# Optimization experiments

Measured on AMD Instinct MI355X. Metric: run time of the kernel, lower is better.

Reference implementation:

```python
import jax, jax.numpy as jnp
import numpy as np

E, TOPK, R = 8, 2, 16          # num_experts, top_k, rank_per_expert
D, H, GH = 1024, 16, 256       # embed_dim, num_heads, gating hidden
HD = D // H
SCALE = HD ** -0.5


def setup_inputs() -> dict:
    key = jax.random.key(0)
    ks = jax.random.split(key, 32)
    B, S = 32, 257
    inp = {"hidden_states": jax.random.normal(ks[0], (B, S, D), jnp.float32)}
    # gating network params
    inp["gw1"] = jax.random.normal(ks[1], (GH, D), jnp.float32) * 0.02
    inp["gb1"] = jnp.zeros((GH,), jnp.float32)
    inp["gw2"] = jax.random.normal(ks[2], (E, GH), jnp.float32) * 0.02
    inp["gb2"] = jnp.zeros((E,), jnp.float32)
    # four SVDMoeLinear projections: main weight, expert U/S/V, bias
    i = 3
    for p in ("q", "k", "v", "o"):
        inp[p + "Wm"] = jax.random.normal(ks[i], (D, D), jnp.float32) * 0.02; i += 1
        inp[p + "U"] = jax.random.normal(ks[i], (E, D, R), jnp.float32) * 0.02; i += 1
        inp[p + "S"] = jax.random.normal(ks[i], (E, R), jnp.float32) * 0.1; i += 1
        inp[p + "V"] = jax.random.normal(ks[i], (E, R, D), jnp.float32) * 0.02; i += 1
        inp[p + "b"] = jnp.zeros((D,), jnp.float32)
    return inp


def _svd_moe(x, Wm, U, S, V, b, idx, gates):
    # x: (B,S,D); idx,gates: (B,k); U:(E,D,R) S:(E,R) V:(E,R,D)
    main = jnp.einsum('bsd,od->bso', x, Wm)
    Ug, Sg, Vg = U[idx], S[idx], V[idx]        # (B,k,D,R), (B,k,R), (B,k,R,D)
    xv = jnp.einsum('bsd,bkrd->bksr', x, Vg)   # project into expert subspace
    xvs = xv * Sg[:, :, None, :]
    eo = jnp.einsum('bksr,bkor->bkso', xvs, Ug)
    expert = jnp.einsum('bkso,bk->bso', eo, gates)
    return main + expert + b


def reference(hidden_states, gw1, gb1, gw2, gb2,
              qWm, qU, qS, qV, qb,
              kWm, kU, kS, kV, kb,
              vWm, vU, vS, vV, vb,
              oWm, oU, oS, oV, ob):
    B, S, _ = hidden_states.shape
    # per-sample gating on pooled features
    pooled = hidden_states.mean(axis=1)
    h = jax.nn.relu(pooled @ gw1.T + gb1)
    logits = h @ gw2.T + gb2                    # (B,E)
    top_vals, top_idx = jax.lax.top_k(logits, TOPK)
    gates = jax.nn.softmax(top_vals, axis=-1)   # (B,k)

    q = _svd_moe(hidden_states, qWm, qU, qS, qV, qb, top_idx, gates) * SCALE
    k = _svd_moe(hidden_states, kWm, kU, kS, kV, kb, top_idx, gates)
    v = _svd_moe(hidden_states, vWm, vU, vS, vV, vb, top_idx, gates)

    def shp(t):
        return t.reshape(B, S, H, HD).transpose(0, 2, 1, 3)  # (B,H,S,HD)
    q, k, v = shp(q), shp(k), shp(v)
    attn = jax.nn.softmax(jnp.einsum('bhsd,bhtd->bhst', q, k), axis=-1)
    ctx = jnp.einsum('bhst,bhtd->bhsd', attn, v)
    ctx = ctx.transpose(0, 2, 1, 3).reshape(B, S, D)
    out = _svd_moe(ctx, oWm, oU, oS, oV, ob, top_idx, gates)
    return out
```

## Files before the change

kernel.cpp:

```cpp
#include <hip/hip_runtime.h>
#include <math.h>

#define Bb   32
#define SQ   257
#define SQV  320
#define Dm   1024
#define HD   64
#define Ee   8
#define Rr   16
#define GHh  256
#define NT   (Bb*SQ)
#define KX   1152
#define LDP  72

typedef unsigned short ush;
typedef _Float16 h16;
typedef __attribute__((ext_vector_type(8))) _Float16 half8;
typedef __attribute__((ext_vector_type(4))) _Float16 half4;
typedef __attribute__((ext_vector_type(8))) short short8;
typedef __attribute__((ext_vector_type(4))) float floatx4;
typedef __attribute__((ext_vector_type(16))) float floatx16;

__device__ __forceinline__ ush f2h(float f) {
    union { h16 h; ush u; } a; a.h = (h16)f; return a.u;
}
__device__ __forceinline__ void store_h4(ush* p, float4 v) {
    half4 h; h.x = (h16)v.x; h.y = (h16)v.y; h.z = (h16)v.z; h.w = (h16)v.w;
    *(half4*)p = h;
}
__device__ __forceinline__ void load16(const ush* g, ush* l) {
    __builtin_amdgcn_global_load_lds(
        (const __attribute__((address_space(1))) unsigned int*)g,
        (__attribute__((address_space(3))) unsigned int*)l,
        16, 0, 0);
}

__global__ __launch_bounds__(256) void prep_kernel(
    const float* __restrict__ x, float* __restrict__ pp, ush* __restrict__ xf,
    const float* __restrict__ W0, const float* __restrict__ U0,
    const float* __restrict__ W1, const float* __restrict__ U1,
    const float* __restrict__ W2, const float* __restrict__ U2,
    const float* __restrict__ W3, const float* __restrict__ U3,
    const float* __restrict__ V0, const float* __restrict__ V1,
    const float* __restrict__ V2, const float* __restrict__ V3,
    ush* __restrict__ Bf0, ush* __restrict__ Bf1,
    ush* __restrict__ Bf2, ush* __restrict__ Bf3,
    ush* __restrict__ Vf)
{
    const int bid = blockIdx.x, t = threadIdx.x;
    if (bid < 512) {
        const int c = bid & 15, b = bid >> 4;
        const int s0 = c * 16, s1 = (c == 15) ? SQ : s0 + 16;
        float4 acc = make_float4(0.f, 0.f, 0.f, 0.f);
        const float* xp = x + ((size_t)b * SQ + s0) * Dm + t * 4;
        ush* xo = xf + ((size_t)b * SQ + s0) * Dm + t * 4;
        for (int s = s0; s < s1; ++s, xp += Dm, xo += Dm) {
            float4 v = *(const float4*)xp;
            store_h4(xo, v);
            acc.x += v.x; acc.y += v.y; acc.z += v.z; acc.w += v.w;
        }
        *(float4*)(pp + ((size_t)b * 16 + c) * Dm + t * 4) = acc;
        return;
    }
    const int bx = bid - 512;
    const int p = bx / 1280, xb = bx % 1280;
    if (xb < 1152) {
        const float* W = p == 0 ? W0 : p == 1 ? W1 : p == 2 ? W2 : W3;
        const float* U = p == 0 ? U0 : p == 1 ? U1 : p == 2 ? U2 : U3;
        ush* Bf = p == 0 ? Bf0 : p == 1 ? Bf1 : p == 2 ? Bf2 : Bf3;
        const int i = xb * 256 + t;
        const int n = i / 288, c4 = i % 288, col = c4 * 4;
        float4 v;
        if (col < Dm) {
            v = *(const float4*)(W + (size_t)n * Dm + col);
        } else {
            int ec = col - Dm, e = ec >> 4, r = ec & 15;
            v = *(const float4*)(U + ((size_t)(e * Dm + n)) * Rr + r);
        }
        store_h4(Bf + (size_t)n * KX + col, v);
    } else {
        const float* V = p == 0 ? V0 : p == 1 ? V1 : p == 2 ? V2 : V3;
        const size_t i = ((size_t)(xb - 1152) * 256 + t) * 4;
        float4 v = *(const float4*)(V + i);
        store_h4(Vf + (size_t)p * Ee * Rr * Dm + i, v);
    }
}

__global__ __launch_bounds__(256) void gating_h(
    const float* __restrict__ pp, const float* __restrict__ gw1,
    const float* __restrict__ gb1, float* __restrict__ hbufg)
{
    __shared__ float pooled[Dm];
    const int b = blockIdx.x, slice = blockIdx.y, t = threadIdx.x;
    const int w = t >> 6, lane = t & 63;

    float4 acc = make_float4(0.f, 0.f, 0.f, 0.f);
    for (int c = 0; c < 16; ++c) {
        float4 v = *(const float4*)(pp + ((size_t)b * 16 + c) * Dm + t * 4);
        acc.x += v.x; acc.y += v.y; acc.z += v.z; acc.w += v.w;
    }
    const float sc = 1.0f / SQ;
    pooled[t*4+0] = acc.x * sc; pooled[t*4+1] = acc.y * sc;
    pooled[t*4+2] = acc.z * sc; pooled[t*4+3] = acc.w * sc;
    __syncthreads();

    for (int oi = 0; oi < 16; ++oi) {
        const int o = slice * 64 + w * 16 + oi;
        const float* g = gw1 + (size_t)o * Dm;
        float s = 0.f;
        #pragma unroll
        for (int i = 0; i < 16; ++i) s += pooled[lane + i*64] * g[lane + i*64];
        for (int off = 32; off > 0; off >>= 1) s += __shfl_down(s, off, 64);
        if (lane == 0) hbufg[b * GHh + o] = fmaxf(s + gb1[o], 0.f);
    }
}

__global__ __launch_bounds__(64) void gating_top(
    const float* __restrict__ hbufg, const float* __restrict__ gw2,
    const float* __restrict__ gb2,
    float* __restrict__ gates, int* __restrict__ idx)
{
    __shared__ float logits[Ee];
    const int b = blockIdx.x, t = threadIdx.x;
    if (t < Ee) {
        const float* g = gw2 + t * GHh;
        const float* hb = hbufg + b * GHh;
        float s = 0.f;
        for (int j = 0; j < GHh; ++j) s += hb[j] * g[j];
        logits[t] = s + gb2[t];
    }
    __syncthreads();
    if (t == 0) {
        int i1 = 0; float v1 = logits[0];
        for (int e = 1; e < Ee; ++e) if (logits[e] > v1) { v1 = logits[e]; i1 = e; }
        int i2 = 0; float v2 = -1e30f;
        for (int e = 0; e < Ee; ++e) if (e != i1 && logits[e] > v2) { v2 = logits[e]; i2 = e; }
        float e2 = __expf(v2 - v1);
        float inv = 1.f / (1.f + e2);
        gates[b*2+0] = inv; gates[b*2+1] = e2 * inv;
        idx[b*2+0] = i1; idx[b*2+1] = i2;
    }
}

template<int NP>
__global__ __launch_bounds__(256) void ext_gemm(
    const ush* __restrict__ xf,
    const ush* __restrict__ Vf,
    const float* __restrict__ S0, const float* __restrict__ S1,
    const float* __restrict__ S2,
    ush* __restrict__ o0, ush* __restrict__ o1, ush* __restrict__ o2,
    const float* __restrict__ gates, const int* __restrict__ idx, int pbase)
{
    __shared__ ush sA[2*64*32], sB[2*NP*16*32];
    const int mt = blockIdx.x, b = blockIdx.y, kk = blockIdx.z;
    const int t = threadIdx.x, lane = t & 63, w = t >> 6;
    const int quad = lane >> 4, l16 = lane & 15;
    const int s0 = mt * 64;
    const int e = idx[b*2+kk];
    const float g = gates[b*2+kk];

    if (kk == 0) {
        const int e0 = idx[b*2+0], e1 = idx[b*2+1];
        int zexp[6]; int nz = 0;
        #pragma unroll
        for (int ez = 0; ez < Ee; ++ez)
            if (ez != e0 && ez != e1) zexp[nz++] = ez;
        short8 zv = {0,0,0,0,0,0,0,0};
        for (int u = t; u < NP*64*6; u += 256) {
            const int ei = u % 6; int rest = u / 6;
            const int r64 = rest & 63; const int p = rest >> 6;
            const int s = s0 + r64;
            if (s < SQ) {
                ush* oo = p == 0 ? o0 : p == 1 ? o1 : o2;
                ush* dst = oo + ((size_t)(b*SQ + s)) * 128 + zexp[ei]*16;
                *(short8*)dst = zv;
                *(short8*)(dst + 8) = zv;
            }
        }
    }

    const int rl = lane >> 2;
    const int swsrc = ((lane & 3) ^ ((lane >> 3) & 3)) * 8;
    const int swrd  = ((quad ^ ((l16 >> 1) & 3)) * 8);

    int sa = s0 + w * 16 + rl; if (sa > SQ - 1) sa = SQ - 1;
    const ush* aptr = xf + ((size_t)(b * SQ + sa)) * Dm + swsrc;
    const ush* bptr = (w < NP)
        ? Vf + ((size_t)(pbase + w)) * Ee * Rr * Dm + ((size_t)(e * Rr + rl)) * Dm + swsrc
        : nullptr;
    ush* la0 = &sA[w * 512];
    ush* la1 = &sA[2048 + w * 512];
    ush* lb0 = (w < NP) ? &sB[w * 512] : nullptr;
    ush* lb1 = (w < NP) ? &sB[NP*512 + w * 512] : nullptr;

    floatx4 S[NP] = {};

    for (int it = 0; it < 16; ++it) {
        __syncthreads();
        load16(aptr, la0); load16(aptr + 32, la1); aptr += 64;
        if (w < NP) {
            load16(bptr, lb0); load16(bptr + 32, lb1); bptr += 64;
        }
        __syncthreads();
        #pragma unroll
        for (int j = 0; j < 2; ++j) {
            const half8 a = *(const half8*)&sA[j*2048 + (w*16 + l16)*32 + swrd];
            #pragma unroll
            for (int p = 0; p < NP; ++p) {
                const half8 bb = *(const half8*)&sB[j*NP*512 + (p*16 + l16)*32 + swrd];
                S[p] = __builtin_amdgcn_mfma_f32_16x16x32_f16(a, bb, S[p], 0, 0, 0);
            }
        }
    }

    #pragma unroll
    for (int p = 0; p < NP; ++p) {
        const float* Sp = p == 0 ? S0 : p == 1 ? S1 : S2;
        const float scale = g * Sp[e * Rr + l16];
        ush* oo = p == 0 ? o0 : p == 1 ? o1 : o2;
        #pragma unroll
        for (int r = 0; r < 4; ++r) {
            const int s = s0 + w * 16 + quad * 4 + r;
            if (s < SQ)
                oo[((size_t)(b * SQ + s)) * 128 + e * 16 + l16] = f2h(S[p][r] * scale);
        }
    }
}

template<int MODE>
__global__ __launch_bounds__(256) void gemm_mfma(
    const ush* __restrict__ A,
    const ush* __restrict__ E0, const ush* __restrict__ E1, const ush* __restrict__ E2,
    const ush* __restrict__ B0, const ush* __restrict__ B1, const ush* __restrict__ B2,
    const float* __restrict__ b0, const float* __restrict__ b1, const float* __restrict__ b2,
    ush* __restrict__ y0, ush* __restrict__ y1, ush* __restrict__ vt,
    float* __restrict__ yo, float qscale)
{
    const int stripe = blockIdx.x % 72;
    if (stripe >= 65) return;
    const int nb = blockIdx.x / 72;
    const int z = blockIdx.z;
    const ush* E = z == 0 ? E0 : z == 1 ? E1 : E2;
    const ush* Bm = z == 0 ? B0 : z == 1 ? B1 : B2;
    const float* bias = z == 0 ? b0 : z == 1 ? b1 : b2;

    __shared__ ush sLDS[2*128*64];
    ush* sA = sLDS;
    ush* sB = sLDS + 128*64;
    const int t = threadIdx.x, lane = t & 63, w = t >> 6;
    const int m0 = stripe * 128, n0 = nb * 128;
    const int row8 = lane >> 3, c8l = lane & 7;
    const int swk = (c8l ^ row8) * 8;
    const int wm = w >> 1, wn = w & 1;
    const int l31 = lane & 31, h5 = lane >> 5;

    const ush* ap[4]; const ush* ep[4]; const ush* bp[4];
    ush *la[4], *lb[4];
    #pragma unroll
    for (int c = 0; c < 4; ++c) {
        const int j = c * 4 + w;
        const int rowl = j * 8 + row8;
        int rga = m0 + rowl; if (rga > NT - 1) rga = NT - 1;
        ap[c] = A + (size_t)rga * Dm + swk;
        ep[c] = E + (size_t)rga * 128 + swk;
        bp[c] = Bm + (size_t)(n0 + rowl) * KX + swk;
        la[c] = &sA[j * 512];
        lb[c] = &sB[j * 512];
    }

    int aofs[4][2], bofs[4][2];
    #pragma unroll
    for (int s = 0; s < 4; ++s)
        #pragma unroll
        for (int i = 0; i < 2; ++i) {
            const int g = s * 2 + h5;
            aofs[s][i] = (wm*64 + i*32 + l31) * 64 + ((g ^ (l31 & 7)) * 8);
            bofs[s][i] = (wn*64 + i*32 + l31) * 64 + ((g ^ (l31 & 7)) * 8);
        }

    floatx16 acc[2][2] = {};

    for (int it = 0; it < 16; ++it) {
        __syncthreads();
        #pragma unroll
        for (int c = 0; c < 4; ++c) {
            load16(ap[c], la[c]); ap[c] += 64;
            load16(bp[c], lb[c]); bp[c] += 64;
        }
        __syncthreads();
        #pragma unroll
        for (int s = 0; s < 4; ++s) {
            half8 af0 = *(const half8*)&sA[aofs[s][0]];
            half8 af1 = *(const half8*)&sA[aofs[s][1]];
            half8 bf0 = *(const half8*)&sB[bofs[s][0]];
            half8 bf1 = *(const half8*)&sB[bofs[s][1]];
            acc[0][0] = __builtin_amdgcn_mfma_f32_32x32x16_f16(af0, bf0, acc[0][0], 0, 0, 0);
            acc[0][1] = __builtin_amdgcn_mfma_f32_32x32x16_f16(af0, bf1, acc[0][1], 0, 0, 0);
            acc[1][0] = __builtin_amdgcn_mfma_f32_32x32x16_f16(af1, bf0, acc[1][0], 0, 0, 0);
            acc[1][1] = __builtin_amdgcn_mfma_f32_32x32x16_f16(af1, bf1, acc[1][1], 0, 0, 0);
        }
    }
    for (int it = 0; it < 2; ++it) {
        __syncthreads();
        #pragma unroll
        for (int c = 0; c < 4; ++c) {
            load16(ep[c], la[c]); ep[c] += 64;
            load16(bp[c], lb[c]); bp[c] += 64;
        }
        __syncthreads();
        #pragma unroll
        for (int s = 0; s < 4; ++s) {
            half8 af0 = *(const half8*)&sA[aofs[s][0]];
            half8 af1 = *(const half8*)&sA[aofs[s][1]];
            half8 bf0 = *(const half8*)&sB[bofs[s][0]];
            half8 bf1 = *(const half8*)&sB[bofs[s][1]];
            acc[0][0] = __builtin_amdgcn_mfma_f32_32x32x16_f16(af0, bf0, acc[0][0], 0, 0, 0);
            acc[0][1] = __builtin_amdgcn_mfma_f32_32x32x16_f16(af0, bf1, acc[0][1], 0, 0, 0);
            acc[1][0] = __builtin_amdgcn_mfma_f32_32x32x16_f16(af1, bf0, acc[1][0], 0, 0, 0);
            acc[1][1] = __builtin_amdgcn_mfma_f32_32x32x16_f16(af1, bf1, acc[1][1], 0, 0, 0);
        }
    }

    if (MODE == 1) {
        #pragma unroll
        for (int mi = 0; mi < 2; ++mi) {
            #pragma unroll
            for (int ni = 0; ni < 2; ++ni) {
                const int col = n0 + wn*64 + ni*32 + l31;
                const float bsv = bias[col];
                const int rb = m0 + wm*64 + mi*32 + 4*h5;
                #pragma unroll
                for (int r = 0; r < 16; ++r) {
                    const int row = rb + (r & 3) + 8 * (r >> 2);
                    if (row < NT)
                        yo[(size_t)row * Dm + col] = acc[mi][ni][r] + bsv;
                }
            }
        }
    } else {
        __syncthreads();
        #pragma unroll
        for (int mi = 0; mi < 2; ++mi) {
            #pragma unroll
            for (int ni = 0; ni < 2; ++ni) {
                const int colL = wn*64 + ni*32 + l31;
                const float bsv = bias[n0 + colL];
                const int rbL = wm*64 + mi*32 + 4*h5;
                #pragma unroll
                for (int r = 0; r < 16; ++r) {
                    const int rowL = rbL + (r & 3) + 8 * (r >> 2);
                    float val = acc[mi][ni][r] + bsv;
                    if (z == 0) val *= qscale;
                    sLDS[rowL*128 + ((((colL>>3) ^ (rowL&7)) << 3) | (colL & 7))] = f2h(val);
                }
            }
        }
        __syncthreads();
        if (z != 2) {
            ush* y = (z == 0) ? y0 : y1;
            #pragma unroll
            for (int i = 0; i < 8; ++i) {
                const int u = i*256 + t;
                const int rowL = u >> 4, cj = u & 15;
                const int row = m0 + rowL;
                if (row < NT) {
                    half8 v = *(const half8*)&sLDS[rowL*128 + ((cj ^ (rowL&7)) << 3)];
                    *(half8*)(y + (size_t)row * Dm + n0 + cj*8) = v;
                }
            }
        } else {
            #pragma unroll
            for (int i = 0; i < 8; ++i) {
                const int u = i*256 + t;
                const int oct = u & 15, colL = u >> 4;
                const int colg = n0 + colL;
                const int h_ = colg >> 6, d_ = colg & 63;
                const size_t vrow = (size_t)h_ * 64 + d_;
                #pragma unroll
                for (int jj = 0; jj < 8; ++jj) {
                    const int rowL = oct + jj*16;
                    const int row = m0 + rowL;
                    if (row < NT) {
                        const int b_ = row / SQ, s_ = row - b_*SQ;
                        vt[((size_t)b_*1024 + vrow) * SQV + s_] =
                            sLDS[rowL*128 + ((((colL>>3) ^ (rowL&7)) << 3) | (colL & 7))];
                    }
                }
            }
        }
    }
}

__global__ __launch_bounds__(256) void attn_mfma(
    const ush* __restrict__ q, const ush* __restrict__ k,
    const ush* __restrict__ vt, ush* __restrict__ cf)
{
    __shared__ ush sK[64*LDP], sVt[64*LDP];
    __shared__ ush sP[4][16*LDP];
    const int qt = blockIdx.x, h = blockIdx.y, b = blockIdx.z;
    const int t = threadIdx.x, lane = t & 63, w = t >> 6;
    const int quad = lane >> 4, l16 = lane & 15;
    const size_t base = (size_t)b * SQ * Dm + (size_t)h * HD;
    const size_t vbase = ((size_t)(b * 16 + h)) * 64 * SQV;

    #pragma unroll
    for (int i = 0; i < 2; ++i) {
        const int u = t + i * 256;
        const int row = u >> 3, c8 = u & 7;
        int s = qt * 64 + row; if (s > SQ - 1) s = SQ - 1;
        short8 ld = *(const short8*)(q + base + (size_t)s * Dm + c8 * 8);
        *(short8*)&sK[row*LDP + c8*8] = ld;
    }
    __syncthreads();
    half8 qf[2];
    #pragma unroll
    for (int s = 0; s < 2; ++s)
        qf[s] = *(const half8*)&sK[(w*16 + l16)*LDP + s*32 + quad*8];

    floatx4 O[4] = {};
    float mrow[4], lrow[4];
    #pragma unroll
    for (int r = 0; r < 4; ++r) { mrow[r] = -1e30f; lrow[r] = 0.f; }
    const bool active = (qt * 64 + w * 16) < SQ;

    short8 kreg[2], vreg[2];
    auto prefetch = [&](int kt) {
        #pragma unroll
        for (int i = 0; i < 2; ++i) {
            const int u = t + i * 256;
            const int row = u >> 3, c8 = u & 7;
            const int s = kt * 64 + row;
            short8 kv = {0,0,0,0,0,0,0,0};
            if (s < SQ) kv = *(const short8*)(k + base + (size_t)s * Dm + c8 * 8);
            kreg[i] = kv;
            vreg[i] = *(const short8*)(vt + vbase + (size_t)row * SQV + kt*64 + c8*8);
        }
    };
    prefetch(0);

    for (int kt = 0; kt < 5; ++kt) {
        __syncthreads();
        #pragma unroll
        for (int i = 0; i < 2; ++i) {
            const int u = t + i * 256;
            const int row = u >> 3, c8 = u & 7;
            *(short8*)&sK[row*LDP + c8*8] = kreg[i];
            *(short8*)&sVt[row*LDP + c8*8] = vreg[i];
        }
        if (kt < 4) prefetch(kt + 1);
        __syncthreads();
        if (!active) continue;

        floatx4 S[4] = {};
        #pragma unroll
        for (int ni = 0; ni < 4; ++ni)
            #pragma unroll
            for (int s = 0; s < 2; ++s) {
                half8 kf = *(const half8*)&sK[(ni*16 + l16)*LDP + s*32 + quad*8];
                S[ni] = __builtin_amdgcn_mfma_f32_16x16x32_f16(qf[s], kf, S[ni], 0, 0, 0);
            }
        #pragma unroll
        for (int ni = 0; ni < 4; ++ni) {
            const int jg = kt * 64 + ni * 16 + l16;
            if (jg >= SQ) { S[ni][0] = -1e30f; S[ni][1] = -1e30f; S[ni][2] = -1e30f; S[ni][3] = -1e30f; }
        }
        float mnew[4], alpha[4];
        #pragma unroll
        for (int r = 0; r < 4; ++r) {
            float mx = fmaxf(fmaxf(S[0][r], S[1][r]), fmaxf(S[2][r], S[3][r]));
            #pragma unroll
            for (int off = 1; off < 16; off <<= 1) mx = fmaxf(mx, __shfl_xor(mx, off, 64));
            mnew[r] = fmaxf(mrow[r], mx);
            alpha[r] = __expf(mrow[r] - mnew[r]);
            mrow[r] = mnew[r];
        }
        float p[4][4], rs[4];
        #pragma unroll
        for (int r = 0; r < 4; ++r) rs[r] = 0.f;
        #pragma unroll
        for (int ni = 0; ni < 4; ++ni)
            #pragma unroll
            for (int r = 0; r < 4; ++r) {
                float e = __expf(S[ni][r] - mnew[r]);
                p[ni][r] = e; rs[r] += e;
            }
        #pragma unroll
        for (int r = 0; r < 4; ++r) {
            #pragma unroll
            for (int off = 1; off < 16; off <<= 1) rs[r] += __shfl_xor(rs[r], off, 64);
            lrow[r] = lrow[r] * alpha[r] + rs[r];
        }
        #pragma unroll
        for (int ni = 0; ni < 4; ++ni)
            #pragma unroll
            for (int r = 0; r < 4; ++r) O[ni][r] *= alpha[r];
        #pragma unroll
        for (int ni = 0; ni < 4; ++ni)
            #pragma unroll
            for (int r = 0; r < 4; ++r)
                sP[w][(quad*4 + r)*LDP + ni*16 + l16] = f2h(p[ni][r]);
        #pragma unroll
        for (int ni = 0; ni < 4; ++ni)
            #pragma unroll
            for (int s = 0; s < 2; ++s) {
                half8 a  = *(const half8*)&sP[w][l16*LDP + s*32 + quad*8];
                half8 bb = *(const half8*)&sVt[(ni*16 + l16)*LDP + s*32 + quad*8];
                O[ni] = __builtin_amdgcn_mfma_f32_16x16x32_f16(a, bb, O[ni], 0, 0, 0);
            }
    }

    if (active) {
        #pragma unroll
        for (int ni = 0; ni < 4; ++ni) {
            const int col = h * HD + ni * 16 + l16;
            #pragma unroll
            for (int r = 0; r < 4; ++r) {
                const int s = qt * 64 + w * 16 + quad * 4 + r;
                if (s < SQ)
                    cf[((size_t)(b * SQ + s)) * Dm + col] = f2h(O[ni][r] / lrow[r]);
            }
        }
    }
}

extern "C" void kernel_launch(void* const* d_in, const int* in_sizes, int n_in,
                              void* d_out, int out_size, void* d_ws, size_t ws_size,
                              hipStream_t stream)
{
    const float* x   = (const float*)d_in[0];
    const float* gw1 = (const float*)d_in[1];
    const float* gb1 = (const float*)d_in[2];
    const float* gw2 = (const float*)d_in[3];
    const float* gb2 = (const float*)d_in[4];
    const float *Wm[4], *U[4], *Sv[4], *Vv[4], *bias[4];
    for (int p = 0; p < 4; ++p) {
        Wm[p]   = (const float*)d_in[5 + p*5 + 0];
        U[p]    = (const float*)d_in[5 + p*5 + 1];
        Sv[p]   = (const float*)d_in[5 + p*5 + 2];
        Vv[p]   = (const float*)d_in[5 + p*5 + 3];
        bias[p] = (const float*)d_in[5 + p*5 + 4];
    }
    char* wsb   = (char*)d_ws;
    float* gates = (float*)wsb;
    int*   idx   = (int*)(wsb + 256);
    float* pool  = (float*)(wsb + 1024);
    float* hbufg = (float*)(wsb + 1024 + (size_t)Bb * 16 * Dm * 4);
    ush* p = (ush*)(wsb + 1024 + (size_t)Bb * 16 * Dm * 4 + (size_t)Bb * GHh * 4);
    ush* xf = p; p += (size_t)NT * Dm;
    ush* ef[4];
    for (int i = 0; i < 4; ++i) { ef[i] = p; p += (size_t)NT * 128; }
    ush* Bf[4];
    for (int i = 0; i < 4; ++i) { Bf[i] = p; p += (size_t)1024 * KX; }
    ush* Vf = p; p += (size_t)4 * Ee * Rr * Dm;
    ush* qf = p; p += (size_t)NT * Dm;
    ush* kf = p; p += (size_t)NT * Dm;
    ush* vt = p; p += (size_t)Bb * 16 * 64 * SQV;

    prep_kernel<<<5632, 256, 0, stream>>>(
        x, pool, xf,
        Wm[0], U[0], Wm[1], U[1], Wm[2], U[2], Wm[3], U[3],
        Vv[0], Vv[1], Vv[2], Vv[3],
        Bf[0], Bf[1], Bf[2], Bf[3], Vf);
    gating_h<<<dim3(Bb, 4), 256, 0, stream>>>(pool, gw1, gb1, hbufg);
    gating_top<<<Bb, 64, 0, stream>>>(hbufg, gw2, gb2, gates, idx);

    ext_gemm<3><<<dim3(5, Bb, 2), 256, 0, stream>>>(xf, Vf,
        Sv[0], Sv[1], Sv[2], ef[0], ef[1], ef[2], gates, idx, 0);

    gemm_mfma<0><<<dim3(576, 1, 3), 256, 0, stream>>>(
        xf, ef[0], ef[1], ef[2], Bf[0], Bf[1], Bf[2],
        bias[0], bias[1], bias[2], qf, kf, vt, nullptr, 0.125f);

    attn_mfma<<<dim3(5, 16, Bb), 256, 0, stream>>>(qf, kf, vt, xf);

    ext_gemm<1><<<dim3(5, Bb, 2), 256, 0, stream>>>(xf, Vf,
        Sv[3], Sv[3], Sv[3], ef[3], ef[3], ef[3], gates, idx, 3);

    gemm_mfma<1><<<dim3(576, 1, 1), 256, 0, stream>>>(
        xf, ef[3], ef[3], ef[3], Bf[3], Bf[3], Bf[3],
        bias[3], bias[3], bias[3], nullptr, nullptr, nullptr, (float*)d_out, 1.0f);
}
```

Baseline: 349.2 us.

## Load attention K/V fragments directly from global memory, drop LDS staging

```diff
diff --git a/kernel.cpp b/kernel.cpp
--- a/kernel.cpp
+++ b/kernel.cpp
@@ -104,8 +104,8 @@
     pooled[t*4+2] = acc.z * sc; pooled[t*4+3] = acc.w * sc;
     __syncthreads();
 
-    for (int oi = 0; oi < 16; ++oi) {
-        const int o = slice * 64 + w * 16 + oi;
+    for (int oi = 0; oi < 8; ++oi) {
+        const int o = slice * 32 + w * 8 + oi;
         const float* g = gw1 + (size_t)o * Dm;
         float s = 0.f;
         #pragma unroll
@@ -395,7 +395,6 @@
     const ush* __restrict__ q, const ush* __restrict__ k,
     const ush* __restrict__ vt, ush* __restrict__ cf)
 {
-    __shared__ ush sK[64*LDP], sVt[64*LDP];
     __shared__ ush sP[4][16*LDP];
     const int qt = blockIdx.x, h = blockIdx.y, b = blockIdx.z;
     const int t = threadIdx.x, lane = t & 63, w = t >> 6;
@@ -403,62 +402,34 @@
     const size_t base = (size_t)b * SQ * Dm + (size_t)h * HD;
     const size_t vbase = ((size_t)(b * 16 + h)) * 64 * SQV;
 
-    #pragma unroll
-    for (int i = 0; i < 2; ++i) {
-        const int u = t + i * 256;
-        const int row = u >> 3, c8 = u & 7;
-        int s = qt * 64 + row; if (s > SQ - 1) s = SQ - 1;
-        short8 ld = *(const short8*)(q + base + (size_t)s * Dm + c8 * 8);
-        *(short8*)&sK[row*LDP + c8*8] = ld;
-    }
-    __syncthreads();
+    if (qt * 64 + w * 16 >= SQ) return;
+
     half8 qf[2];
-    #pragma unroll
-    for (int s = 0; s < 2; ++s)
-        qf[s] = *(const half8*)&sK[(w*16 + l16)*LDP + s*32 + quad*8];
+    {
+        int r = qt * 64 + w * 16 + l16; if (r > SQ - 1) r = SQ - 1;
+        const ush* qp = q + base + (size_t)r * Dm;
+        #pragma unroll
+        for (int s = 0; s < 2; ++s)
+            qf[s] = *(const half8*)(qp + s * 32 + quad * 8);
+    }
 
     floatx4 O[4] = {};
     float mrow[4], lrow[4];
     #pragma unroll
     for (int r = 0; r < 4; ++r) { mrow[r] = -1e30f; lrow[r] = 0.f; }
-    const bool active = (qt * 64 + w * 16) < SQ;
-
-    short8 kreg[2], vreg[2];
-    auto prefetch = [&](int kt) {
-        #pragma unroll
-        for (int i = 0; i < 2; ++i) {
-            const int u = t + i * 256;
-            const int row = u >> 3, c8 = u & 7;
-            const int s = kt * 64 + row;
-            short8 kv = {0,0,0,0,0,0,0,0};
-            if (s < SQ) kv = *(const short8*)(k + base + (size_t)s * Dm + c8 * 8);
-            kreg[i] = kv;
-            vreg[i] = *(const short8*)(vt + vbase + (size_t)row * SQV + kt*64 + c8*8);
-        }
-    };
-    prefetch(0);
 
     for (int kt = 0; kt < 5; ++kt) {
-        __syncthreads();
-        #pragma unroll
-        for (int i = 0; i < 2; ++i) {
-            const int u = t + i * 256;
-            const int row = u >> 3, c8 = u & 7;
-            *(short8*)&sK[row*LDP + c8*8] = kreg[i];
-            *(short8*)&sVt[row*LDP + c8*8] = vreg[i];
-        }
-        if (kt < 4) prefetch(kt + 1);
-        __syncthreads();
-        if (!active) continue;
-
         floatx4 S[4] = {};
         #pragma unroll
-        for (int ni = 0; ni < 4; ++ni)
+        for (int ni = 0; ni < 4; ++ni) {
+            int kr = kt * 64 + ni * 16 + l16; if (kr > SQ - 1) kr = SQ - 1;
+            const ush* kp = k + base + (size_t)kr * Dm;
             #pragma unroll
             for (int s = 0; s < 2; ++s) {
-                half8 kf = *(const half8*)&sK[(ni*16 + l16)*LDP + s*32 + quad*8];
+                half8 kf = *(const half8*)(kp + s * 32 + quad * 8);
                 S[ni] = __builtin_amdgcn_mfma_f32_16x16x32_f16(qf[s], kf, S[ni], 0, 0, 0);
             }
+        }
         #pragma unroll
         for (int ni = 0; ni < 4; ++ni) {
             const int jg = kt * 64 + ni * 16 + l16;
@@ -500,25 +471,25 @@
             for (int r = 0; r < 4; ++r)
                 sP[w][(quad*4 + r)*LDP + ni*16 + l16] = f2h(p[ni][r]);
         #pragma unroll
-        for (int ni = 0; ni < 4; ++ni)
+        for (int ni = 0; ni < 4; ++ni) {
+            const ush* vp = vt + vbase + (size_t)(ni*16 + l16) * SQV + kt * 64;
             #pragma unroll
             for (int s = 0; s < 2; ++s) {
                 half8 a  = *(const half8*)&sP[w][l16*LDP + s*32 + quad*8];
-                half8 bb = *(const half8*)&sVt[(ni*16 + l16)*LDP + s*32 + quad*8];
+                half8 bb = *(const half8*)(vp + s*32 + quad*8);
                 O[ni] = __builtin_amdgcn_mfma_f32_16x16x32_f16(a, bb, O[ni], 0, 0, 0);
             }
-    }
-
-    if (active) {
-        #pragma unroll
-        for (int ni = 0; ni < 4; ++ni) {
-            const int col = h * HD + ni * 16 + l16;
-            #pragma unroll
-            for (int r = 0; r < 4; ++r) {
-                const int s = qt * 64 + w * 16 + quad * 4 + r;
-                if (s < SQ)
-                    cf[((size_t)(b * SQ + s)) * Dm + col] = f2h(O[ni][r] / lrow[r]);
-            }
+        }
+    }
+
+    #pragma unroll
+    for (int ni = 0; ni < 4; ++ni) {
+        const int col = h * HD + ni * 16 + l16;
+        #pragma unroll
+        for (int r = 0; r < 4; ++r) {
+            const int s = qt * 64 + w * 16 + quad * 4 + r;
+            if (s < SQ)
+                cf[((size_t)(b * SQ + s)) * Dm + col] = f2h(O[ni][r] / lrow[r]);
         }
     }
 }
@@ -561,7 +532,7 @@
         Wm[0], U[0], Wm[1], U[1], Wm[2], U[2], Wm[3], U[3],
         Vv[0], Vv[1], Vv[2], Vv[3],
         Bf[0], Bf[1], Bf[2], Bf[3], Vf);
-    gating_h<<<dim3(Bb, 4), 256, 0, stream>>>(pool, gw1, gb1, hbufg);
+    gating_h<<<dim3(Bb, 8), 256, 0, stream>>>(pool, gw1, gb1, hbufg);
     gating_top<<<Bb, 64, 0, stream>>>(hbufg, gw2, gb2, gates, idx);
 
     ext_gemm<3><<<dim3(5, Bb, 2), 256, 0, stream>>>(xf, Vf,
```

After: 389.9 us. 1.12x slower.
